# Kernel tuning notes

Hardware: AMD Instinct MI355X
Metric: run time of the kernel (lower is better)

## Reference

```python
import jax, jax.numpy as jnp
import numpy as np

RADIUS = [3, 3, 4, 4]
DILATION = [1, 2, 1, 2]
N_HEAD = 4
D_K = 8
SCALE = 1.0 / np.sqrt(8.0)  # module hardcodes sqrt(8)


def _patches(a, r, d):
    # a: (b, t, c, h, w) -> (b, t, c, ls2, h, w), dilated (2r+1)x(2r+1) window,
    # zero padding (invalid positions masked separately).
    b, t, c, h, w = a.shape
    p = r * d
    ap = jnp.pad(a, ((0, 0), (0, 0), (0, 0), (p, p), (p, p)))
    ls = 2 * r + 1
    sl = [ap[..., dy * d:dy * d + h, dx * d:dx * d + w]
          for dy in range(ls) for dx in range(ls)]
    return jnp.stack(sl, axis=3)


def _valid_mask(h, w, r, d):
    # (ls2, h, w) bool: True where window position is inside the image
    m = _patches(jnp.ones((1, 1, 1, h, w)), r, d)
    return m[0, 0, 0] > 0.5


def _head_attn(q, k, v, r, d):
    # q,k,v: (b, t, c, h, w); attention over all t' frames x local window
    b, t, c, h, w = q.shape
    kp = _patches(k, r, d)        # (b, t', c, p, h, w)
    vp = _patches(v, r, d)
    valid = _valid_mask(h, w, r, d)  # (p, h, w)
    e = jnp.einsum('btchw,bscphw->btsphw', q, kp) * SCALE
    e = jnp.where(valid[None, None, None], e, -jnp.inf)  # OOB -> -inf like CUDA kernel
    e = e.reshape(b, t, t * valid.shape[0], h, w)
    attn = jax.nn.softmax(e, axis=2).reshape(b, t, t, -1, h, w)
    return jnp.einsum('btsphw,bscphw->btchw', attn, vp)


def setup_inputs() -> dict:
    key = jax.random.key(0)
    kx, kq, kk, kv, ko = jax.random.split(key, 5)
    C = 32
    std = 1.0 / np.sqrt(C)
    x = jax.random.normal(kx, (2, 5, C, 64, 64), dtype=jnp.float32)
    Wq = jax.random.normal(kq, (N_HEAD * D_K, C), dtype=jnp.float32) * std
    Wk = jax.random.normal(kk, (N_HEAD * D_K, C), dtype=jnp.float32) * std
    Wv = jax.random.normal(kv, (N_HEAD * D_K, C), dtype=jnp.float32) * std
    Wo = jax.random.normal(ko, (C, C), dtype=jnp.float32) * std
    return {"x": x, "Wq": Wq, "Wk": Wk, "Wv": Wv, "Wo": Wo}


def reference(x, Wq, Wk, Wv, Wo):
    # 1x1x1 Conv3d == per-pixel channel matmul
    q = jnp.einsum('btchw,kc->btkhw', x, Wq)
    k = jnp.einsum('btchw,kc->btkhw', x, Wk)
    v = jnp.einsum('btchw,kc->btkhw', x, Wv)
    outs = []
    for i in range(N_HEAD):
        s = slice(i * D_K, (i + 1) * D_K)
        outs.append(_head_attn(q[:, :, s], k[:, :, s], v[:, :, s],
                               RADIUS[i], DILATION[i]))
    out = jnp.concatenate(outs, axis=2)
    out = jnp.einsum('btchw,kc->btkhw', out, Wo)
    return out + x
```

## Files before the change

### kernel.cpp

```cpp
#include <hip/hip_runtime.h>
#include <stdint.h>

#define NT 5
#define NC 32
#define NH 4
#define HW 4096
#define NPIX 40960
#define QS 0.51006972789f
#define EBIAS 12.0f
#define NINF (-__builtin_inff())

typedef _Float16 half_t;
typedef half_t h2 __attribute__((ext_vector_type(2)));

static __device__ __forceinline__ h2 as_h2(uint32_t u) {
  union { uint32_t u; h2 h; } c; c.u = u; return c.h;
}
static __device__ __forceinline__ uint32_t pack_h2(float a, float b) {
  union { h2 h; uint32_t u; } c;
  c.h.x = (half_t)a; c.h.y = (half_t)b;
  return c.u;
}

#if __has_builtin(__builtin_amdgcn_exp2f)
#define EXP2(x) __builtin_amdgcn_exp2f(x)
#else
#define EXP2(x) exp2f(x)
#endif

static __device__ __forceinline__ float dot8i(const uint4& a, const uint4& b, float c) {
#if __has_builtin(__builtin_amdgcn_fdot2)
  c = __builtin_amdgcn_fdot2(as_h2(a.x), as_h2(b.x), c, false);
  c = __builtin_amdgcn_fdot2(as_h2(a.y), as_h2(b.y), c, false);
  c = __builtin_amdgcn_fdot2(as_h2(a.z), as_h2(b.z), c, false);
  c = __builtin_amdgcn_fdot2(as_h2(a.w), as_h2(b.w), c, false);
  return c;
#else
  const h2 a0 = as_h2(a.x), a1 = as_h2(a.y), a2 = as_h2(a.z), a3 = as_h2(a.w);
  const h2 b0 = as_h2(b.x), b1 = as_h2(b.y), b2 = as_h2(b.z), b3 = as_h2(b.w);
  c = fmaf((float)a0.x, (float)b0.x, c);
  c = fmaf((float)a0.y, (float)b0.y, c);
  c = fmaf((float)a1.x, (float)b1.x, c);
  c = fmaf((float)a1.y, (float)b1.y, c);
  c = fmaf((float)a2.x, (float)b2.x, c);
  c = fmaf((float)a2.y, (float)b2.y, c);
  c = fmaf((float)a3.x, (float)b3.x, c);
  c = fmaf((float)a3.y, (float)b3.y, c);
  return c;
#endif
}

__global__ __launch_bounds__(256) void qkv_kernel(
    const float* __restrict__ x,
    const float* __restrict__ Wq, const float* __restrict__ Wk,
    const float* __restrict__ Wv,
    uint2* __restrict__ qf, uint2* __restrict__ kf, uint2* __restrict__ vf)
{
  const int p   = blockIdx.x * 256 + threadIdx.x;
  const int by  = blockIdx.y;
  const int h   = by >> 1;
  const int jg  = by & 1;
  const int bt  = p >> 12;
  const int pix = p & 4095;

  const float* xp = x + (size_t)bt * (NC * HW) + pix;
  float xc[NC];
  #pragma unroll
  for (int c = 0; c < NC; ++c) xc[c] = xp[(size_t)c * HW];

  float qv[4], kv4[4], vv4[4];
  #pragma unroll
  for (int j = 0; j < 4; ++j) {
    const int o = h * 8 + jg * 4 + j;
    float aq = 0.f, ak = 0.f, av = 0.f;
    #pragma unroll
    for (int c = 0; c < NC; ++c) {
      const float xv = xc[c];
      aq = fmaf(xv, Wq[o * NC + c], aq);
      ak = fmaf(xv, Wk[o * NC + c], ak);
      av = fmaf(xv, Wv[o * NC + c], av);
    }
    qv[j] = aq * QS; kv4[j] = ak; vv4[j] = av;
  }
  const size_t base = (((size_t)bt * NH + h) * HW + pix) * 2 + jg;
  uint2 qq, kk, vv;
  qq.x = pack_h2(qv[0], qv[1]);  qq.y = pack_h2(qv[2], qv[3]);
  kk.x = pack_h2(kv4[0], kv4[1]); kk.y = pack_h2(kv4[2], kv4[3]);
  vv.x = pack_h2(vv4[0], vv4[1]); vv.y = pack_h2(vv4[2], vv4[3]);
  qf[base] = qq;
  kf[base] = kk;
  vf[base] = vv;
}

template <int R, int D>
static __device__ __forceinline__ void attn_body(
    int b, int t, int h, int s, int yb,
    const uint4* __restrict__ qf, const uint4* __restrict__ kf,
    const uint4* __restrict__ vf,
    uint4* __restrict__ pa, float* __restrict__ pl,
    uint4* __restrict__ k_lds, uint4* __restrict__ v_lds)
{
  constexpr int LS    = 2 * R + 1;
  constexpr int NROWS = 8 + 2 * R;
  const int tid  = threadIdx.x;
  const int w    = tid >> 6;
  const int lane = tid & 63;

  const int y0 = (D == 1) ? (yb * 8) : ((yb & 1) + 2 * ((yb >> 1) * 8));

  const uint4* kg = kf + (size_t)((b * NT + s) * NH + h) * HW;
  const uint4* vg = vf + (size_t)((b * NT + s) * NH + h) * HW;
  for (int idx = tid; idx < NROWS * 64; idx += 256) {
    const int r  = idx >> 6, xs = idx & 63;
    int ys = y0 + (r - R) * D;
    ys = ys < 0 ? 0 : (ys > 63 ? 63 : ys);
    const int pos = (D == 1) ? xs : ((xs & 1) * 32 + (xs >> 1));
    k_lds[r * 64 + pos] = kg[ys * 64 + xs];
    v_lds[r * 64 + pos] = vg[ys * 64 + xs];
  }
  __syncthreads();

  const int xp = lane >> 5;
  const int cb = (D == 1) ? lane : (lane & 31);
  const int x  = (D == 1) ? lane : (2 * (lane & 31) + xp);
  const int yA = y0 + 2 * w * D;
  const int yB = yA + D;
  const int pixA = yA * 64 + x, pixB = yB * 64 + x;

  const uint4* qp = qf + (size_t)((b * NT + t) * NH + h) * HW;
  const uint4 qA = qp[pixA];
  const uint4 qB = qp[pixB];

  int   posArr[LS];
  float eoArr[LS];
  #pragma unroll
  for (int i = 0; i < LS; ++i) {
    const int  cx  = cb + i - R;
    const bool okx = (unsigned)cx < (D == 1 ? 64u : 32u);
    const int  cc  = okx ? cx : 0;
    posArr[i] = (D == 1) ? cc : (xp * 32 + cc);
    eoArr[i]  = okx ? 0.f : NINF;
  }

  float lA = 0.f, lB = 0.f;
  h2 aA[4], aB[4];
  const h2 z2 = { (half_t)0.f, (half_t)0.f };
  #pragma unroll
  for (int i = 0; i < 4; ++i) { aA[i] = z2; aB[i] = z2; }

  #pragma unroll 2
  for (int u = 0; u <= LS; ++u) {
    const int ykey = y0 + (2 * w + u - R) * D;
    const bool oky = (unsigned)ykey < 64u;
    const bool okA = (u < LS) && oky;
    const bool okB = (u > 0)  && oky;
    if (!(okA || okB)) continue;
    const float biA = okA ? -EBIAS : NINF;
    const float biB = okB ? -EBIAS : NINF;
    const uint4* kr = k_lds + (2 * w + u) * 64;
    const uint4* vr = v_lds + (2 * w + u) * 64;

    uint4 kbuf[2], vbuf[2];
    #pragma unroll
    for (int i = 0; i < 2; ++i) {
      kbuf[i] = kr[posArr[i]];
      vbuf[i] = vr[posArr[i]];
    }
    #pragma unroll
    for (int i = 0; i < LS; ++i) {
      const uint4 kk = kbuf[i & 1];
      const uint4 vv = vbuf[i & 1];
      if (i + 2 < LS) {
        kbuf[i & 1] = kr[posArr[i + 2]];
        vbuf[i & 1] = vr[posArr[i + 2]];
      }
      const float ciA = biA + eoArr[i];
      const float ciB = biB + eoArr[i];
      const float pA = EXP2(dot8i(qA, kk, ciA));
      const float pB = EXP2(dot8i(qB, kk, ciB));
      lA += pA; lB += pB;
      const half_t pAh = (half_t)pA, pBh = (half_t)pB;
      const h2 pA2 = { pAh, pAh }, pB2 = { pBh, pBh };
      const h2 w0 = as_h2(vv.x), w1 = as_h2(vv.y), w2 = as_h2(vv.z), w3 = as_h2(vv.w);
      aA[0] += pA2 * w0; aA[1] += pA2 * w1; aA[2] += pA2 * w2; aA[3] += pA2 * w3;
      aB[0] += pB2 * w0; aB[1] += pB2 * w1; aB[2] += pB2 * w2; aB[3] += pB2 * w3;
    }
  }

  const size_t plane = (size_t)(s * NH + h) * NPIX + (size_t)(b * NT + t) * HW;
  union { h2 hh[4]; uint4 u; } cA, cB;
  #pragma unroll
  for (int i = 0; i < 4; ++i) { cA.hh[i] = aA[i]; cB.hh[i] = aB[i]; }
  pa[plane + pixA] = cA.u;
  pa[plane + pixB] = cB.u;
  pl[plane + pixA] = lA;
  pl[plane + pixB] = lB;
}

__global__ __launch_bounds__(256) void attn_kernel(
    const uint4* __restrict__ qf, const uint4* __restrict__ kf,
    const uint4* __restrict__ vf, uint4* __restrict__ pa, float* __restrict__ pl)
{
  __shared__ uint4 k_lds[16 * 64];
  __shared__ uint4 v_lds[16 * 64];
  const int bid = blockIdx.x;
  int h, rest;
  if (bid < 800) { h = 2 + (bid & 1); rest = bid >> 1; }
  else           { h = ((bid - 800) & 1); rest = (bid - 800) >> 1; }
  const int yb = rest & 7; rest >>= 3;
  const int s  = rest % 5;
  const int bt = rest / 5;
  const int t = bt % NT, b = bt / NT;
  if      (h == 0) attn_body<3, 1>(b, t, 0, s, yb, qf, kf, vf, pa, pl, k_lds, v_lds);
  else if (h == 1) attn_body<3, 2>(b, t, 1, s, yb, qf, kf, vf, pa, pl, k_lds, v_lds);
  else if (h == 2) attn_body<4, 1>(b, t, 2, s, yb, qf, kf, vf, pa, pl, k_lds, v_lds);
  else             attn_body<4, 2>(b, t, 3, s, yb, qf, kf, vf, pa, pl, k_lds, v_lds);
}

__global__ __launch_bounds__(256) void reduce_kernel(
    const uint4* __restrict__ pa, const float* __restrict__ pl,
    uint4* __restrict__ of)
{
  const int p = blockIdx.x * 256 + threadIdx.x;
  const int h = blockIdx.y;

  float a[8], l = 0.f;
  #pragma unroll
  for (int i = 0; i < 8; ++i) a[i] = 0.f;
  #pragma unroll
  for (int s = 0; s < NT; ++s) {
    const size_t plane = (size_t)(s * NH + h) * NPIX + p;
    const uint4 v = pa[plane];
    l += pl[plane];
    const h2 v0 = as_h2(v.x), v1 = as_h2(v.y), v2 = as_h2(v.z), v3 = as_h2(v.w);
    a[0] += (float)v0.x; a[1] += (float)v0.y;
    a[2] += (float)v1.x; a[3] += (float)v1.y;
    a[4] += (float)v2.x; a[5] += (float)v2.y;
    a[6] += (float)v3.x; a[7] += (float)v3.y;
  }
  const float inv = 1.0f / l;
  uint4 r;
  r.x = pack_h2(a[0] * inv, a[1] * inv);
  r.y = pack_h2(a[2] * inv, a[3] * inv);
  r.z = pack_h2(a[4] * inv, a[5] * inv);
  r.w = pack_h2(a[6] * inv, a[7] * inv);
  of[(size_t)h * NPIX + p] = r;
}

__global__ __launch_bounds__(256) void proj_kernel(
    const uint4* __restrict__ of, const float* __restrict__ x,
    const float* __restrict__ Wo, float* __restrict__ out)
{
  const int p   = blockIdx.x * 256 + threadIdx.x;
  const int og  = blockIdx.y;
  const int bt  = p >> 12;
  const int pix = p & 4095;

  float oc[32];
  #pragma unroll
  for (int h = 0; h < NH; ++h) {
    const uint4 v = of[(size_t)h * NPIX + p];
    const h2 v0 = as_h2(v.x), v1 = as_h2(v.y), v2 = as_h2(v.z), v3 = as_h2(v.w);
    oc[h * 8 + 0] = (float)v0.x; oc[h * 8 + 1] = (float)v0.y;
    oc[h * 8 + 2] = (float)v1.x; oc[h * 8 + 3] = (float)v1.y;
    oc[h * 8 + 4] = (float)v2.x; oc[h * 8 + 5] = (float)v2.y;
    oc[h * 8 + 6] = (float)v3.x; oc[h * 8 + 7] = (float)v3.y;
  }

  const float* xpt = x + (size_t)bt * (NC * HW) + pix;
  float* yp = out + (size_t)bt * (NC * HW) + pix;
  #pragma unroll
  for (int oo = 0; oo < 4; ++oo) {
    const int o = og * 4 + oo;
    float acc = xpt[(size_t)o * HW];
    #pragma unroll
    for (int c = 0; c < NC; ++c)
      acc = fmaf(oc[c], Wo[o * NC + c], acc);
    yp[(size_t)o * HW] = acc;
  }
}

extern "C" void kernel_launch(void* const* d_in, const int* in_sizes, int n_in,
                              void* d_out, int out_size, void* d_ws, size_t ws_size,
                              hipStream_t stream)
{
  const float* x  = (const float*)d_in[0];
  const float* Wq = (const float*)d_in[1];
  const float* Wk = (const float*)d_in[2];
  const float* Wv = (const float*)d_in[3];
  const float* Wo = (const float*)d_in[4];

  char* ws = (char*)d_ws;
  uint2* qf = (uint2*)ws;
  uint2* kf = (uint2*)(ws + 2621440);
  uint2* vf = (uint2*)(ws + 2 * 2621440);
  uint4* pa = (uint4*)(ws + 3 * 2621440);
  float* pl = (float*)(ws + 3 * 2621440 + 13107200);
  uint4* of = (uint4*)(ws + 3 * 2621440 + 13107200 + 3276800);

  qkv_kernel<<<dim3(160, 8), 256, 0, stream>>>(x, Wq, Wk, Wv, qf, kf, vf);
  attn_kernel<<<1600, 256, 0, stream>>>((const uint4*)qf, (const uint4*)kf,
                                        (const uint4*)vf, pa, pl);
  reduce_kernel<<<dim3(160, 4), 256, 0, stream>>>((const uint4*)pa, pl, of);
  proj_kernel<<<dim3(160, 8), 256, 0, stream>>>((const uint4*)of, x, Wo,
                                                (float*)d_out);
}
```

Baseline: 110.6 us.

## Compute two horizontally adjacent pixels per thread to reuse LDS K/V loads

Each thread now handles 2x2 pixels (two adjacent columns in two rows) instead of one column in two rows, and the block shrinks from 256 to 128 threads. Each window row loads LS+1 K/V entries from LDS once into registers and shares them between the two column neighbours, roughly halving LDS traffic per output. The cost is higher register pressure from four accumulator sets and the full K/V buffers, fewer threads per block, and loss of the previous software-pipelined LDS prefetch.

```diff
diff --git a/kernel.cpp b/kernel.cpp
--- a/kernel.cpp
+++ b/kernel.cpp
@@ -102,6 +102,7 @@
 {
   constexpr int LS    = 2 * R + 1;
   constexpr int NROWS = 8 + 2 * R;
+  constexpr int CMAX  = (D == 1) ? 64 : 32;
   const int tid  = threadIdx.x;
   const int w    = tid >> 6;
   const int lane = tid & 63;
@@ -110,7 +111,7 @@
 
   const uint4* kg = kf + (size_t)((b * NT + s) * NH + h) * HW;
   const uint4* vg = vf + (size_t)((b * NT + s) * NH + h) * HW;
-  for (int idx = tid; idx < NROWS * 64; idx += 256) {
+  for (int idx = tid; idx < NROWS * 64; idx += 128) {
     const int r  = idx >> 6, xs = idx & 63;
     int ys = y0 + (r - R) * D;
     ys = ys < 0 ? 0 : (ys > 63 ? 63 : ys);
@@ -120,84 +121,100 @@
   }
   __syncthreads();
 
-  const int xp = lane >> 5;
-  const int cb = (D == 1) ? lane : (lane & 31);
-  const int x  = (D == 1) ? lane : (2 * (lane & 31) + xp);
-  const int yA = y0 + 2 * w * D;
+  const int rp  = (D == 1) ? (2 * w + (lane >> 5)) : (2 * w + ((lane >> 4) & 1));
+  const int xp  = (D == 1) ? 0 : (lane >> 5);
+  const int j   = (D == 1) ? (lane & 31) : (lane & 15);
+  const int cc0 = 2 * j;
+
+  const int x0 = (D == 1) ? cc0 : (2 * cc0 + xp);
+  const int x1 = (D == 1) ? (cc0 + 1) : (2 * (cc0 + 1) + xp);
+
+  const int yA = y0 + 2 * rp * D;
   const int yB = yA + D;
-  const int pixA = yA * 64 + x, pixB = yB * 64 + x;
+  const int pixA0 = yA * 64 + x0, pixA1 = yA * 64 + x1;
+  const int pixB0 = yB * 64 + x0, pixB1 = yB * 64 + x1;
 
   const uint4* qp = qf + (size_t)((b * NT + t) * NH + h) * HW;
-  const uint4 qA = qp[pixA];
-  const uint4 qB = qp[pixB];
-
-  int   posArr[LS];
-  float eoArr[LS];
-  #pragma unroll
-  for (int i = 0; i < LS; ++i) {
-    const int  cx  = cb + i - R;
-    const bool okx = (unsigned)cx < (D == 1 ? 64u : 32u);
+  const uint4 qA0 = qp[pixA0], qA1 = qp[pixA1];
+  const uint4 qB0 = qp[pixB0], qB1 = qp[pixB1];
+
+  int   posArr[LS + 1];
+  float eoArr[LS + 1];
+  #pragma unroll
+  for (int i = 0; i <= LS; ++i) {
+    const int  cx  = cc0 - R + i;
+    const bool okx = (unsigned)cx < (unsigned)CMAX;
     const int  cc  = okx ? cx : 0;
     posArr[i] = (D == 1) ? cc : (xp * 32 + cc);
     eoArr[i]  = okx ? 0.f : NINF;
   }
 
-  float lA = 0.f, lB = 0.f;
-  h2 aA[4], aB[4];
+  float lA0 = 0.f, lA1 = 0.f, lB0 = 0.f, lB1 = 0.f;
+  h2 aA0[4], aA1[4], aB0[4], aB1[4];
   const h2 z2 = { (half_t)0.f, (half_t)0.f };
   #pragma unroll
-  for (int i = 0; i < 4; ++i) { aA[i] = z2; aB[i] = z2; }
-
-  #pragma unroll 2
+  for (int i = 0; i < 4; ++i) { aA0[i] = z2; aA1[i] = z2; aB0[i] = z2; aB1[i] = z2; }
+
+  #pragma unroll 1
   for (int u = 0; u <= LS; ++u) {
-    const int ykey = y0 + (2 * w + u - R) * D;
+    const int ykey = y0 + (2 * rp + u - R) * D;
     const bool oky = (unsigned)ykey < 64u;
     const bool okA = (u < LS) && oky;
     const bool okB = (u > 0)  && oky;
     if (!(okA || okB)) continue;
     const float biA = okA ? -EBIAS : NINF;
     const float biB = okB ? -EBIAS : NINF;
-    const uint4* kr = k_lds + (2 * w + u) * 64;
-    const uint4* vr = v_lds + (2 * w + u) * 64;
-
-    uint4 kbuf[2], vbuf[2];
+    const uint4* kr = k_lds + (2 * rp + u) * 64;
+    const uint4* vr = v_lds + (2 * rp + u) * 64;
+
+    uint4 kbuf[LS + 1], vbuf[LS + 1];
     #pragma unroll
-    for (int i = 0; i < 2; ++i) {
+    for (int i = 0; i <= LS; ++i) {
       kbuf[i] = kr[posArr[i]];
       vbuf[i] = vr[posArr[i]];
     }
+
     #pragma unroll
     for (int i = 0; i < LS; ++i) {
-      const uint4 kk = kbuf[i & 1];
-      const uint4 vv = vbuf[i & 1];
-      if (i + 2 < LS) {
-        kbuf[i & 1] = kr[posArr[i + 2]];
-        vbuf[i & 1] = vr[posArr[i + 2]];
-      }
-      const float ciA = biA + eoArr[i];
-      const float ciB = biB + eoArr[i];
-      const float pA = EXP2(dot8i(qA, kk, ciA));
-      const float pB = EXP2(dot8i(qB, kk, ciB));
-      lA += pA; lB += pB;
-      const half_t pAh = (half_t)pA, pBh = (half_t)pB;
-      const h2 pA2 = { pAh, pAh }, pB2 = { pBh, pBh };
-      const h2 w0 = as_h2(vv.x), w1 = as_h2(vv.y), w2 = as_h2(vv.z), w3 = as_h2(vv.w);
-      aA[0] += pA2 * w0; aA[1] += pA2 * w1; aA[2] += pA2 * w2; aA[3] += pA2 * w3;
-      aB[0] += pB2 * w0; aB[1] += pB2 * w1; aB[2] += pB2 * w2; aB[3] += pB2 * w3;
+      const float ciA0 = biA + eoArr[i];
+      const float ciA1 = biA + eoArr[i + 1];
+      const float ciB0 = biB + eoArr[i];
+      const float ciB1 = biB + eoArr[i + 1];
+      const float pA0 = EXP2(dot8i(qA0, kbuf[i],     ciA0));
+      const float pA1 = EXP2(dot8i(qA1, kbuf[i + 1], ciA1));
+      const float pB0 = EXP2(dot8i(qB0, kbuf[i],     ciB0));
+      const float pB1 = EXP2(dot8i(qB1, kbuf[i + 1], ciB1));
+      lA0 += pA0; lA1 += pA1; lB0 += pB0; lB1 += pB1;
+      const half_t hA0 = (half_t)pA0, hA1 = (half_t)pA1;
+      const half_t hB0 = (half_t)pB0, hB1 = (half_t)pB1;
+      const h2 qA0v = { hA0, hA0 }, qA1v = { hA1, hA1 };
+      const h2 qB0v = { hB0, hB0 }, qB1v = { hB1, hB1 };
+      const uint4 v0 = vbuf[i], v1 = vbuf[i + 1];
+      const h2 w00 = as_h2(v0.x), w01 = as_h2(v0.y), w02 = as_h2(v0.z), w03 = as_h2(v0.w);
+      const h2 w10 = as_h2(v1.x), w11 = as_h2(v1.y), w12 = as_h2(v1.z), w13 = as_h2(v1.w);
+      aA0[0] += qA0v * w00; aA0[1] += qA0v * w01; aA0[2] += qA0v * w02; aA0[3] += qA0v * w03;
+      aA1[0] += qA1v * w10; aA1[1] += qA1v * w11; aA1[2] += qA1v * w12; aA1[3] += qA1v * w13;
+      aB0[0] += qB0v * w00; aB0[1] += qB0v * w01; aB0[2] += qB0v * w02; aB0[3] += qB0v * w03;
+      aB1[0] += qB1v * w10; aB1[1] += qB1v * w11; aB1[2] += qB1v * w12; aB1[3] += qB1v * w13;
     }
   }
 
   const size_t plane = (size_t)(s * NH + h) * NPIX + (size_t)(b * NT + t) * HW;
-  union { h2 hh[4]; uint4 u; } cA, cB;
-  #pragma unroll
-  for (int i = 0; i < 4; ++i) { cA.hh[i] = aA[i]; cB.hh[i] = aB[i]; }
-  pa[plane + pixA] = cA.u;
-  pa[plane + pixB] = cB.u;
-  pl[plane + pixA] = lA;
-  pl[plane + pixB] = lB;
-}
-
-__global__ __launch_bounds__(256) void attn_kernel(
+  union { h2 hh[4]; uint4 u; } c0, c1, c2, c3;
+  #pragma unroll
+  for (int i = 0; i < 4; ++i) { c0.hh[i] = aA0[i]; c1.hh[i] = aA1[i];
+                                c2.hh[i] = aB0[i]; c3.hh[i] = aB1[i]; }
+  pa[plane + pixA0] = c0.u;
+  pa[plane + pixA1] = c1.u;
+  pa[plane + pixB0] = c2.u;
+  pa[plane + pixB1] = c3.u;
+  pl[plane + pixA0] = lA0;
+  pl[plane + pixA1] = lA1;
+  pl[plane + pixB0] = lB0;
+  pl[plane + pixB1] = lB1;
+}
+
+__global__ __launch_bounds__(128) void attn_kernel(
     const uint4* __restrict__ qf, const uint4* __restrict__ kf,
     const uint4* __restrict__ vf, uint4* __restrict__ pa, float* __restrict__ pl)
 {
@@ -299,7 +316,7 @@
   uint4* of = (uint4*)(ws + 3 * 2621440 + 13107200 + 3276800);
 
   qkv_kernel<<<dim3(160, 8), 256, 0, stream>>>(x, Wq, Wk, Wv, qf, kf, vf);
-  attn_kernel<<<1600, 256, 0, stream>>>((const uint4*)qf, (const uint4*)kf,
+  attn_kernel<<<1600, 128, 0, stream>>>((const uint4*)qf, (const uint4*)kf,
                                         (const uint4*)vf, pa, pl);
   reduce_kernel<<<dim3(160, 4), 256, 0, stream>>>((const uint4*)pa, pl, of);
   proj_kernel<<<dim3(160, 8), 256, 0, stream>>>((const uint4*)of, x, Wo,
```

Result: slower. 120.9 us (+9.3%).
